# Kernel tuning notes

Measured on AMD Instinct MI355X. Metric: run time of the kernel, lower is better.

The kernel has to match this reference:

```python
import jax, jax.numpy as jnp
import numpy as np

N = 10000
E = 320000
D_IN = 512
D_OUT = 256


def setup_inputs() -> dict:
    key = jax.random.key(0)
    ks = jax.random.split(key, 10)
    x = jax.random.normal(ks[0], (N, D_IN), dtype=jnp.float32)
    edge_index = jax.random.randint(ks[1], (2, E), 0, N, dtype=jnp.int64)
    s_in = 1.0 / np.sqrt(D_IN)
    s_out = 1.0 / np.sqrt(D_OUT)
    W0 = jax.random.uniform(ks[2], (D_IN, D_OUT), minval=-s_in, maxval=s_in, dtype=jnp.float32)
    b0 = jax.random.uniform(ks[3], (D_OUT,), minval=-s_in, maxval=s_in, dtype=jnp.float32)
    Wl1 = jax.random.uniform(ks[4], (D_OUT, D_OUT), minval=-s_out, maxval=s_out, dtype=jnp.float32)
    bl1 = jax.random.uniform(ks[5], (D_OUT,), minval=-s_out, maxval=s_out, dtype=jnp.float32)
    Wr1 = jax.random.uniform(ks[6], (D_OUT, D_OUT), minval=-s_out, maxval=s_out, dtype=jnp.float32)
    Wl2 = jax.random.uniform(ks[7], (D_OUT, D_OUT), minval=-s_out, maxval=s_out, dtype=jnp.float32)
    bl2 = jax.random.uniform(ks[8], (D_OUT,), minval=-s_out, maxval=s_out, dtype=jnp.float32)
    Wr2 = jax.random.uniform(ks[9], (D_OUT, D_OUT), minval=-s_out, maxval=s_out, dtype=jnp.float32)
    return {"x": x, "edge_index": edge_index, "W0": W0, "b0": b0,
            "Wl1": Wl1, "bl1": bl1, "Wr1": Wr1,
            "Wl2": Wl2, "bl2": bl2, "Wr2": Wr2}


def _sage_conv(h, src, dst, Wl, bl, Wr):
    # mean aggregation over incoming edges: msg j->i uses h[src], summed at dst
    msg = h[src]                                        # [E, D]
    agg = jax.ops.segment_sum(msg, dst, num_segments=N)  # [N, D]
    deg = jax.ops.segment_sum(jnp.ones((msg.shape[0],), h.dtype), dst, num_segments=N)
    mean = agg / jnp.maximum(deg, 1.0)[:, None]
    return mean @ Wl + bl + h @ Wr


def reference(x, edge_index, W0, b0, Wl1, bl1, Wr1, Wl2, bl2, Wr2):
    src, dst = edge_index[0], edge_index[1]
    h = x @ W0 + b0                 # lin; dropout = identity (eval mode)
    out1 = jax.nn.relu(_sage_conv(h, src, dst, Wl1, bl1, Wr1)) + h
    out2 = _sage_conv(out1, src, dst, Wl2, bl2, Wr2) + out1
    return (out1, out2)
```

## Files before the change

### kernel.cpp

```cpp
#include <hip/hip_runtime.h>
#include <cstdint>

#define N_NODES 10000
#define N_EDGES 320000
#define DIN 512
#define DOUT 256
#define DEG_CAP 96

using short8 = __attribute__((ext_vector_type(8))) short;
using f32x4  = __attribute__((ext_vector_type(4))) float;
typedef unsigned short ushort_t;

static __device__ __forceinline__ unsigned short f2bf(float f) {
  unsigned u = __builtin_bit_cast(unsigned, f);
  u += 0x7fffu + ((u >> 16) & 1u);
  return (unsigned short)(u >> 16);
}
static __device__ __forceinline__ float bf2f(unsigned short s) {
  unsigned u = ((unsigned)s) << 16;
  return __builtin_bit_cast(float, u);
}

static __device__ __forceinline__ int detect64(const unsigned* ei) {
  unsigned z = 0;
  #pragma unroll
  for (int i = 1; i < 32; i += 2) z |= ei[i];
  return z == 0u;
}
static __device__ __forceinline__ int load_idx(const unsigned* ei, int i, int is64) {
  return is64 ? (int)ei[2 * i] : (int)ei[i];
}

#define B_EDGE 1250
#define B_W    1536
#define B_X    5000
__global__ __launch_bounds__(256) void prep_all(
    const unsigned* __restrict__ ei, int* __restrict__ cnt,
    int* __restrict__ srcs,
    const float* __restrict__ x, ushort_t* __restrict__ xb,
    const float* __restrict__ W0,
    const float* __restrict__ Wl1, const float* __restrict__ Wr1,
    const float* __restrict__ Wl2, const float* __restrict__ Wr2,
    ushort_t* __restrict__ W0T, ushort_t* __restrict__ WT1,
    ushort_t* __restrict__ WT2) {
  int b = blockIdx.x;
  if (b < B_EDGE) {
    int is64 = detect64(ei);
    int e = b * 256 + threadIdx.x;
    int d = load_idx(ei, N_EDGES + e, is64);
    int s = load_idx(ei, e, is64);
    int pos = atomicAdd(&cnt[d], 1);
    if (pos < DEG_CAP) srcs[d * DEG_CAP + pos] = s;
  } else if (b < B_EDGE + B_W) {
    int g = (b - B_EDGE) * 256 + threadIdx.x;
    int mat = g >> 17;
    int r = g & 131071;
    int n = r >> 9, k = r & 511;
    float v;
    ushort_t* dst;
    if (mat == 0)      { v = W0[k * 256 + n]; dst = W0T; }
    else if (mat == 1) { v = (k < 256) ? Wl1[k * 256 + n] : Wr1[(k - 256) * 256 + n]; dst = WT1; }
    else               { v = (k < 256) ? Wl2[k * 256 + n] : Wr2[(k - 256) * 256 + n]; dst = WT2; }
    dst[r] = f2bf(v);
  } else {
    int g = (b - B_EDGE - B_W) * 256 + threadIdx.x;
    float4 f = *(const float4*)(x + (size_t)g * 4);
    uint2 o;
    o.x = (unsigned)f2bf(f.x) | ((unsigned)f2bf(f.y) << 16);
    o.y = (unsigned)f2bf(f.z) | ((unsigned)f2bf(f.w) << 16);
    *(uint2*)(xb + (size_t)g * 4) = o;
  }
}

__global__ __launch_bounds__(256) void agg_mean(const ushort_t* __restrict__ h,
                                                const int* __restrict__ cnt,
                                                const int* __restrict__ srcs,
                                                ushort_t* __restrict__ mean) {
  int node = blockIdx.x * 4 + (threadIdx.x >> 6);
  int lane = threadIdx.x & 63;
  if (node >= N_NODES) return;
  int deg = cnt[node];
  int d = (deg < DEG_CAP) ? deg : DEG_CAP;
  int beg = node * DEG_CAP;
  int end = beg + d;
  float a0 = 0.f, a1 = 0.f, a2 = 0.f, a3 = 0.f;
  int j = beg;
  for (; j + 8 <= end; j += 8) {
    int4 sa = *(const int4*)(srcs + j);
    int4 sb = *(const int4*)(srcs + j + 4);
    uint2 u0 = *(const uint2*)(h + (size_t)sa.x * 256 + lane * 4);
    uint2 u1 = *(const uint2*)(h + (size_t)sa.y * 256 + lane * 4);
    uint2 u2 = *(const uint2*)(h + (size_t)sa.z * 256 + lane * 4);
    uint2 u3 = *(const uint2*)(h + (size_t)sa.w * 256 + lane * 4);
    uint2 u4 = *(const uint2*)(h + (size_t)sb.x * 256 + lane * 4);
    uint2 u5 = *(const uint2*)(h + (size_t)sb.y * 256 + lane * 4);
    uint2 u6 = *(const uint2*)(h + (size_t)sb.z * 256 + lane * 4);
    uint2 u7 = *(const uint2*)(h + (size_t)sb.w * 256 + lane * 4);
    a0 += bf2f(u0.x & 0xffff) + bf2f(u1.x & 0xffff) + bf2f(u2.x & 0xffff) + bf2f(u3.x & 0xffff);
    a1 += bf2f(u0.x >> 16)    + bf2f(u1.x >> 16)    + bf2f(u2.x >> 16)    + bf2f(u3.x >> 16);
    a2 += bf2f(u0.y & 0xffff) + bf2f(u1.y & 0xffff) + bf2f(u2.y & 0xffff) + bf2f(u3.y & 0xffff);
    a3 += bf2f(u0.y >> 16)    + bf2f(u1.y >> 16)    + bf2f(u2.y >> 16)    + bf2f(u3.y >> 16);
    a0 += bf2f(u4.x & 0xffff) + bf2f(u5.x & 0xffff) + bf2f(u6.x & 0xffff) + bf2f(u7.x & 0xffff);
    a1 += bf2f(u4.x >> 16)    + bf2f(u5.x >> 16)    + bf2f(u6.x >> 16)    + bf2f(u7.x >> 16);
    a2 += bf2f(u4.y & 0xffff) + bf2f(u5.y & 0xffff) + bf2f(u6.y & 0xffff) + bf2f(u7.y & 0xffff);
    a3 += bf2f(u4.y >> 16)    + bf2f(u5.y >> 16)    + bf2f(u6.y >> 16)    + bf2f(u7.y >> 16);
  }
  for (; j + 4 <= end; j += 4) {
    int4 s4 = *(const int4*)(srcs + j);
    uint2 u0 = *(const uint2*)(h + (size_t)s4.x * 256 + lane * 4);
    uint2 u1 = *(const uint2*)(h + (size_t)s4.y * 256 + lane * 4);
    uint2 u2 = *(const uint2*)(h + (size_t)s4.z * 256 + lane * 4);
    uint2 u3 = *(const uint2*)(h + (size_t)s4.w * 256 + lane * 4);
    a0 += bf2f(u0.x & 0xffff) + bf2f(u1.x & 0xffff) + bf2f(u2.x & 0xffff) + bf2f(u3.x & 0xffff);
    a1 += bf2f(u0.x >> 16)    + bf2f(u1.x >> 16)    + bf2f(u2.x >> 16)    + bf2f(u3.x >> 16);
    a2 += bf2f(u0.y & 0xffff) + bf2f(u1.y & 0xffff) + bf2f(u2.y & 0xffff) + bf2f(u3.y & 0xffff);
    a3 += bf2f(u0.y >> 16)    + bf2f(u1.y >> 16)    + bf2f(u2.y >> 16)    + bf2f(u3.y >> 16);
  }
  for (; j < end; ++j) {
    int s0 = srcs[j];
    uint2 u0 = *(const uint2*)(h + (size_t)s0 * 256 + lane * 4);
    a0 += bf2f(u0.x & 0xffff);
    a1 += bf2f(u0.x >> 16);
    a2 += bf2f(u0.y & 0xffff);
    a3 += bf2f(u0.y >> 16);
  }
  float inv = 1.0f / (float)(d > 1 ? d : 1);
  a0 *= inv; a1 *= inv; a2 *= inv; a3 *= inv;
  uint2 o;
  o.x = (unsigned)f2bf(a0) | ((unsigned)f2bf(a1) << 16);
  o.y = (unsigned)f2bf(a2) | ((unsigned)f2bf(a3) << 16);
  *(uint2*)(mean + (size_t)node * 256 + lane * 4) = o;
}

template<int DO_RELU, int HAS_ADD, int HAS_OUTF, int HAS_OUTB, int SPLIT_A>
__global__ __launch_bounds__(256) void gemm_pan(
    const ushort_t* __restrict__ A0, const ushort_t* __restrict__ A1,
    const ushort_t* __restrict__ BT, const float* __restrict__ bias,
    const ushort_t* __restrict__ addB,
    float* __restrict__ outF, ushort_t* __restrict__ outB, int M) {
  __shared__ ushort_t Bs[64 * 520];

  const int bid = blockIdx.x;
  const int sg  = bid >> 5;
  const int r32 = bid & 31;
  const int xt  = (sg << 3) + (r32 & 7);
  const int yt  = r32 >> 3;
  const int xtiles = (M + 127) >> 7;
  if (xt >= xtiles) return;

  const int tid  = threadIdx.x;
  const int lane = tid & 63;
  const int w    = tid >> 6;
  const int bn   = yt * 64;
  const int mbase = xt * 128 + w * 32;

  #pragma unroll
  for (int i = 0; i < 16; ++i) {
    int c = i * 256 + tid;
    int row = c >> 6;
    int c8  = (c & 63) * 8;
    uint4 bv = *(const uint4*)(BT + (size_t)(bn + row) * 512 + c8);
    *(uint4*)&Bs[row * 520 + c8] = bv;
  }
  __syncthreads();

  f32x4 acc[2][4] = {};
  const int mrow = lane & 15;
  const int k8   = (lane >> 4) * 8;

  #pragma unroll
  for (int kt = 0; kt < 512; kt += 32) {
    const ushort_t* Asrc;
    int acol, ald;
    if (SPLIT_A) {
      if (kt < 256) { Asrc = A0; acol = kt; } else { Asrc = A1; acol = kt - 256; }
      ald = 256;
    } else {
      Asrc = A0; acol = kt; ald = 512;
    }
    short8 a[2], b[4];
    #pragma unroll
    for (int s = 0; s < 2; ++s) {
      int row = mbase + s * 16 + mrow;
      a[s] = *(const short8*)(Asrc + (size_t)row * ald + acol + k8);
    }
    #pragma unroll
    for (int ni = 0; ni < 4; ++ni)
      b[ni] = *(const short8*)&Bs[(ni * 16 + mrow) * 520 + kt + k8];
    #pragma unroll
    for (int s = 0; s < 2; ++s)
      #pragma unroll
      for (int ni = 0; ni < 4; ++ni)
        acc[s][ni] = __builtin_amdgcn_mfma_f32_16x16x32_bf16(a[s], b[ni], acc[s][ni], 0, 0, 0);
  }

  const int cq   = lane >> 4;
  const int ccol = lane & 15;
  #pragma unroll
  for (int ni = 0; ni < 4; ++ni) {
    int gcol = bn + ni * 16 + ccol;
    float bv = bias[gcol];
    #pragma unroll
    for (int s = 0; s < 2; ++s) {
      #pragma unroll
      for (int r = 0; r < 4; ++r) {
        int grow = mbase + s * 16 + cq * 4 + r;
        if (grow < M) {
          float v = acc[s][ni][r] + bv;
          if (DO_RELU) v = fmaxf(v, 0.f);
          if (HAS_ADD) v += bf2f(addB[(size_t)grow * DOUT + gcol]);
          if (HAS_OUTF) __builtin_nontemporal_store(v, &outF[(size_t)grow * DOUT + gcol]);
          if (HAS_OUTB) outB[(size_t)grow * DOUT + gcol] = f2bf(v);
        }
      }
    }
  }
}

extern "C" void kernel_launch(void* const* d_in, const int* in_sizes, int n_in,
                              void* d_out, int out_size, void* d_ws, size_t ws_size,
                              hipStream_t stream) {
  const float*    x   = (const float*)d_in[0];
  const unsigned* ei  = (const unsigned*)d_in[1];
  const float*    W0  = (const float*)d_in[2];
  const float*    b0  = (const float*)d_in[3];
  const float*    Wl1 = (const float*)d_in[4];
  const float*    bl1 = (const float*)d_in[5];
  const float*    Wr1 = (const float*)d_in[6];
  const float*    Wl2 = (const float*)d_in[7];
  const float*    bl2 = (const float*)d_in[8];
  const float*    Wr2 = (const float*)d_in[9];

  char* ws = (char*)d_ws;
  size_t off = 0;
  auto alloc = [&](size_t bytes) {
    char* p = ws + off;
    off += (bytes + 255) & ~(size_t)255;
    return p;
  };
  ushort_t* xb  = (ushort_t*)alloc((size_t)N_NODES * 512 * 2);
  ushort_t* hb  = (ushort_t*)alloc((size_t)N_NODES * 256 * 2);
  ushort_t* o1b = (ushort_t*)alloc((size_t)N_NODES * 256 * 2);
  ushort_t* mb  = (ushort_t*)alloc((size_t)N_NODES * 256 * 2);
  ushort_t* W0T = (ushort_t*)alloc(256 * 512 * 2);
  ushort_t* WT1 = (ushort_t*)alloc(256 * 512 * 2);
  ushort_t* WT2 = (ushort_t*)alloc(256 * 512 * 2);
  int* cnt    = (int*)alloc(N_NODES * 4);
  int* srcs   = (int*)alloc((size_t)N_NODES * DEG_CAP * 4);

  float* out1 = (float*)d_out;
  float* out2 = out1 + (size_t)N_NODES * DOUT;

  hipMemsetAsync(cnt, 0, N_NODES * 4, stream);
  prep_all<<<B_EDGE + B_W + B_X, 256, 0, stream>>>(ei, cnt, srcs, x, xb,
                                                   W0, Wl1, Wr1, Wl2, Wr2,
                                                   W0T, WT1, WT2);

  const int GG = 320;
  gemm_pan<0, 0, 0, 1, 0><<<GG, 256, 0, stream>>>(xb, nullptr, W0T, b0, nullptr,
                                                  nullptr, hb, N_NODES);
  agg_mean<<<(N_NODES + 3) / 4, 256, 0, stream>>>(hb, cnt, srcs, mb);
  gemm_pan<1, 1, 1, 1, 1><<<GG, 256, 0, stream>>>(mb, hb, WT1, bl1, hb,
                                                  out1, o1b, N_NODES);
  agg_mean<<<(N_NODES + 3) / 4, 256, 0, stream>>>(o1b, cnt, srcs, mb);
  gemm_pan<0, 1, 1, 0, 1><<<GG, 256, 0, stream>>>(mb, o1b, WT2, bl2, o1b,
                                                  out2, nullptr, N_NODES);
}
```

Baseline: 196.4 us.

## Overlap aggregation with root-weight GEMM and fuse x bf16 conversion into GEMM

Splits each SAGE layer's fused K=512 GEMM into two K=256 GEMMs. The h@Wr+bias half runs in the same launch as the neighbor mean aggregation, so memory-bound gather blocks and MFMA blocks can share the GPU. It also drops the separate x->bf16 pass by converting fp32 x inside the first GEMM's A load. In exchange it adds an fp32 intermediate buffer t that is written and read back each layer, and the first GEMM now loads A in fp32.

```diff
diff --git a/kernel.cpp b/kernel.cpp
--- a/kernel.cpp
+++ b/kernel.cpp
@@ -6,6 +6,7 @@
 #define DIN 512
 #define DOUT 256
 #define DEG_CAP 96
+#define AGGB 2500
 
 using short8 = __attribute__((ext_vector_type(8))) short;
 using f32x4  = __attribute__((ext_vector_type(4))) float;
@@ -33,16 +34,15 @@
 
 #define B_EDGE 1250
 #define B_W    1536
-#define B_X    5000
 __global__ __launch_bounds__(256) void prep_all(
     const unsigned* __restrict__ ei, int* __restrict__ cnt,
     int* __restrict__ srcs,
-    const float* __restrict__ x, ushort_t* __restrict__ xb,
     const float* __restrict__ W0,
     const float* __restrict__ Wl1, const float* __restrict__ Wr1,
     const float* __restrict__ Wl2, const float* __restrict__ Wr2,
-    ushort_t* __restrict__ W0T, ushort_t* __restrict__ WT1,
-    ushort_t* __restrict__ WT2) {
+    ushort_t* __restrict__ W0T,
+    ushort_t* __restrict__ WlT1, ushort_t* __restrict__ WrT1,
+    ushort_t* __restrict__ WlT2, ushort_t* __restrict__ WrT2) {
   int b = blockIdx.x;
   if (b < B_EDGE) {
     int is64 = detect64(ei);
@@ -51,32 +51,27 @@
     int s = load_idx(ei, e, is64);
     int pos = atomicAdd(&cnt[d], 1);
     if (pos < DEG_CAP) srcs[d * DEG_CAP + pos] = s;
-  } else if (b < B_EDGE + B_W) {
+  } else {
     int g = (b - B_EDGE) * 256 + threadIdx.x;
     int mat = g >> 17;
     int r = g & 131071;
     int n = r >> 9, k = r & 511;
-    float v;
-    ushort_t* dst;
-    if (mat == 0)      { v = W0[k * 256 + n]; dst = W0T; }
-    else if (mat == 1) { v = (k < 256) ? Wl1[k * 256 + n] : Wr1[(k - 256) * 256 + n]; dst = WT1; }
-    else               { v = (k < 256) ? Wl2[k * 256 + n] : Wr2[(k - 256) * 256 + n]; dst = WT2; }
-    dst[r] = f2bf(v);
-  } else {
-    int g = (b - B_EDGE - B_W) * 256 + threadIdx.x;
-    float4 f = *(const float4*)(x + (size_t)g * 4);
-    uint2 o;
-    o.x = (unsigned)f2bf(f.x) | ((unsigned)f2bf(f.y) << 16);
-    o.y = (unsigned)f2bf(f.z) | ((unsigned)f2bf(f.w) << 16);
-    *(uint2*)(xb + (size_t)g * 4) = o;
-  }
-}
-
-__global__ __launch_bounds__(256) void agg_mean(const ushort_t* __restrict__ h,
-                                                const int* __restrict__ cnt,
-                                                const int* __restrict__ srcs,
-                                                ushort_t* __restrict__ mean) {
-  int node = blockIdx.x * 4 + (threadIdx.x >> 6);
+    if (mat == 0) {
+      W0T[n * 512 + k] = f2bf(W0[k * 256 + n]);
+    } else if (mat == 1) {
+      if (k < 256) WlT1[n * 256 + k]         = f2bf(Wl1[k * 256 + n]);
+      else         WrT1[n * 256 + (k - 256)] = f2bf(Wr1[(k - 256) * 256 + n]);
+    } else {
+      if (k < 256) WlT2[n * 256 + k]         = f2bf(Wl2[k * 256 + n]);
+      else         WrT2[n * 256 + (k - 256)] = f2bf(Wr2[(k - 256) * 256 + n]);
+    }
+  }
+}
+
+static __device__ __forceinline__ void agg_body(
+    int bid, const ushort_t* __restrict__ h, const int* __restrict__ cnt,
+    const int* __restrict__ srcs, ushort_t* __restrict__ mean) {
+  int node = bid * 4 + (threadIdx.x >> 6);
   int lane = threadIdx.x & 63;
   if (node >= N_NODES) return;
   int deg = cnt[node];
@@ -132,61 +127,67 @@
   *(uint2*)(mean + (size_t)node * 256 + lane * 4) = o;
 }
 
-template<int DO_RELU, int HAS_ADD, int HAS_OUTF, int HAS_OUTB, int SPLIT_A>
-__global__ __launch_bounds__(256) void gemm_pan(
-    const ushort_t* __restrict__ A0, const ushort_t* __restrict__ A1,
-    const ushort_t* __restrict__ BT, const float* __restrict__ bias,
-    const ushort_t* __restrict__ addB,
-    float* __restrict__ outF, ushort_t* __restrict__ outB, int M) {
-  __shared__ ushort_t Bs[64 * 520];
-
-  const int bid = blockIdx.x;
-  const int sg  = bid >> 5;
-  const int r32 = bid & 31;
-  const int xt  = (sg << 3) + (r32 & 7);
-  const int yt  = r32 >> 3;
-  const int xtiles = (M + 127) >> 7;
-  if (xt >= xtiles) return;
-
-  const int tid  = threadIdx.x;
+template<int KDIM, int AF32, int HB, int ADDF, int RELU, int RES,
+         int OUTF, int NTF, int OUTB, int ROT>
+static __device__ __forceinline__ void gemm_body(
+    int gbid, const void* __restrict__ Av, const ushort_t* __restrict__ BT,
+    const float* __restrict__ bias, const float* __restrict__ addF,
+    const ushort_t* __restrict__ resB, float* __restrict__ outF,
+    ushort_t* __restrict__ outB, int M, ushort_t* Bs) {
+  constexpr int LDB = KDIM + 8;
+  const int sg = gbid >> 5, r32 = gbid & 31;
+  const int xt = (sg << 3) + ((r32 + ROT) & 7);
+  const int yt = r32 >> 3;
+  if (xt >= ((M + 127) >> 7)) return;
+  const int tid = threadIdx.x;
   const int lane = tid & 63;
-  const int w    = tid >> 6;
-  const int bn   = yt * 64;
+  const int w = tid >> 6;
+  const int bn = yt * 64;
   const int mbase = xt * 128 + w * 32;
 
+  constexpr int CPR = KDIM / 8;
   #pragma unroll
-  for (int i = 0; i < 16; ++i) {
+  for (int i = 0; i < (64 * CPR) / 256; ++i) {
     int c = i * 256 + tid;
-    int row = c >> 6;
-    int c8  = (c & 63) * 8;
-    uint4 bv = *(const uint4*)(BT + (size_t)(bn + row) * 512 + c8);
-    *(uint4*)&Bs[row * 520 + c8] = bv;
+    int row = c / CPR;
+    int c8 = (c % CPR) * 8;
+    uint4 bv = *(const uint4*)(BT + (size_t)(bn + row) * KDIM + c8);
+    *(uint4*)&Bs[row * LDB + c8] = bv;
   }
   __syncthreads();
 
   f32x4 acc[2][4] = {};
   const int mrow = lane & 15;
-  const int k8   = (lane >> 4) * 8;
+  const int k8 = (lane >> 4) * 8;
 
   #pragma unroll
-  for (int kt = 0; kt < 512; kt += 32) {
-    const ushort_t* Asrc;
-    int acol, ald;
-    if (SPLIT_A) {
-      if (kt < 256) { Asrc = A0; acol = kt; } else { Asrc = A1; acol = kt - 256; }
-      ald = 256;
-    } else {
-      Asrc = A0; acol = kt; ald = 512;
-    }
+  for (int kt = 0; kt < KDIM; kt += 32) {
     short8 a[2], b[4];
     #pragma unroll
     for (int s = 0; s < 2; ++s) {
       int row = mbase + s * 16 + mrow;
-      a[s] = *(const short8*)(Asrc + (size_t)row * ald + acol + k8);
+      if (AF32) {
+        const float* Af = (const float*)Av;
+        float4 f0 = {}, f1 = {};
+        if (row < M) {
+          const float* p = Af + (size_t)row * KDIM + kt + k8;
+          f0 = *(const float4*)p;
+          f1 = *(const float4*)(p + 4);
+        }
+        short8 av;
+        av[0] = (short)f2bf(f0.x); av[1] = (short)f2bf(f0.y);
+        av[2] = (short)f2bf(f0.z); av[3] = (short)f2bf(f0.w);
+        av[4] = (short)f2bf(f1.x); av[5] = (short)f2bf(f1.y);
+        av[6] = (short)f2bf(f1.z); av[7] = (short)f2bf(f1.w);
+        a[s] = av;
+      } else {
+        const ushort_t* Ab = (const ushort_t*)Av;
+        a[s] = *(const short8*)(Ab + (size_t)row * KDIM + kt + k8);
+      }
     }
     #pragma unroll
     for (int ni = 0; ni < 4; ++ni)
-      b[ni] = *(const short8*)&Bs[(ni * 16 + mrow) * 520 + kt + k8];
+      b[ni] = *(const short8*)&Bs[(ni * 16 + mrow) * LDB + kt + k8];
     #pragma unroll
     for (int s = 0; s < 2; ++s)
       #pragma unroll
@@ -194,27 +195,67 @@
         acc[s][ni] = __builtin_amdgcn_mfma_f32_16x16x32_bf16(a[s], b[ni], acc[s][ni], 0, 0, 0);
   }
 
-  const int cq   = lane >> 4;
+  const int cq = lane >> 4;
   const int ccol = lane & 15;
   #pragma unroll
   for (int ni = 0; ni < 4; ++ni) {
     int gcol = bn + ni * 16 + ccol;
-    float bv = bias[gcol];
+    float bv = HB ? bias[gcol] : 0.f;
     #pragma unroll
     for (int s = 0; s < 2; ++s) {
       #pragma unroll
       for (int r = 0; r < 4; ++r) {
         int grow = mbase + s * 16 + cq * 4 + r;
         if (grow < M) {
-          float v = acc[s][ni][r] + bv;
-          if (DO_RELU) v = fmaxf(v, 0.f);
-          if (HAS_ADD) v += bf2f(addB[(size_t)grow * DOUT + gcol]);
-          if (HAS_OUTF) __builtin_nontemporal_store(v, &outF[(size_t)grow * DOUT + gcol]);
-          if (HAS_OUTB) outB[(size_t)grow * DOUT + gcol] = f2bf(v);
+          size_t idx = (size_t)grow * DOUT + gcol;
+          float v = acc[s][ni][r];
+          if (HB)   v += bv;
+          if (ADDF) v += addF[idx];
+          if (RELU) v = fmaxf(v, 0.f);
+          if (RES)  v += bf2f(resB[idx]);
+          if (OUTF) {
+            if (NTF) __builtin_nontemporal_store(v, &outF[idx]);
+            else     outF[idx] = v;
+          }
+          if (OUTB) outB[idx] = f2bf(v);
         }
       }
     }
   }
+}
+
+__global__ __launch_bounds__(256) void gemm1_k(
+    const float* __restrict__ x, const ushort_t* __restrict__ W0T,
+    const float* __restrict__ b0, ushort_t* __restrict__ hb) {
+  __shared__ ushort_t Bs[64 * 520];
+  gemm_body<512, 1, 1, 0, 0, 0, 0, 0, 1, 0>(blockIdx.x, x, W0T, b0, nullptr,
+                                            nullptr, nullptr, hb, N_NODES, Bs);
+}
+
+__global__ __launch_bounds__(256) void combo_k(
+    const ushort_t* __restrict__ h, const int* __restrict__ cnt,
+    const int* __restrict__ srcs, ushort_t* __restrict__ mean,
+    const ushort_t* __restrict__ BT, const float* __restrict__ bias,
+    float* __restrict__ t) {
+  __shared__ ushort_t Bs[64 * 264];
+  if (blockIdx.x < AGGB) {
+    agg_body(blockIdx.x, h, cnt, srcs, mean);
+  } else {
+    gemm_body<256, 0, 1, 0, 0, 0, 1, 0, 0, 4>(blockIdx.x - AGGB, h, BT, bias,
+                                              nullptr, nullptr, t, nullptr,
+                                              N_NODES, Bs);
+  }
+}
+
+template<int RELU, int OUTB>
+__global__ __launch_bounds__(256) void gemmL_k(
+    const ushort_t* __restrict__ A, const ushort_t* __restrict__ BT,
+    const float* __restrict__ t, const ushort_t* __restrict__ res,
+    float* __restrict__ outF, ushort_t* __restrict__ outB) {
+  __shared__ ushort_t Bs[64 * 264];
+  gemm_body<256, 0, 0, 1, RELU, 1, 1, 1, OUTB, 0>(blockIdx.x, A, BT, nullptr,
+                                                  t, res, outF, outB,
+                                                  N_NODES, Bs);
 }
 
 extern "C" void kernel_launch(void* const* d_in, const int* in_sizes, int n_in,
@@ -238,31 +279,28 @@
     off += (bytes + 255) & ~(size_t)255;
     return p;
   };
-  ushort_t* xb  = (ushort_t*)alloc((size_t)N_NODES * 512 * 2);
-  ushort_t* hb  = (ushort_t*)alloc((size_t)N_NODES * 256 * 2);
-  ushort_t* o1b = (ushort_t*)alloc((size_t)N_NODES * 256 * 2);
-  ushort_t* mb  = (ushort_t*)alloc((size_t)N_NODES * 256 * 2);
-  ushort_t* W0T = (ushort_t*)alloc(256 * 512 * 2);
-  ushort_t* WT1 = (ushort_t*)alloc(256 * 512 * 2);
-  ushort_t* WT2 = (ushort_t*)alloc(256 * 512 * 2);
-  int* cnt    = (int*)alloc(N_NODES * 4);
-  int* srcs   = (int*)alloc((size_t)N_NODES * DEG_CAP * 4);
+  ushort_t* hb   = (ushort_t*)alloc((size_t)N_NODES * 256 * 2);
+  ushort_t* o1b  = (ushort_t*)alloc((size_t)N_NODES * 256 * 2);
+  ushort_t* mb   = (ushort_t*)alloc((size_t)N_NODES * 256 * 2);
+  float*    t    = (float*)   alloc((size_t)N_NODES * 256 * 4);
+  ushort_t* W0T  = (ushort_t*)alloc(256 * 512 * 2);
+  ushort_t* WlT1 = (ushort_t*)alloc(256 * 256 * 2);
+  ushort_t* WrT1 = (ushort_t*)alloc(256 * 256 * 2);
+  ushort_t* WlT2 = (ushort_t*)alloc(256 * 256 * 2);
+  ushort_t* WrT2 = (ushort_t*)alloc(256 * 256 * 2);
+  int* cnt  = (int*)alloc(N_NODES * 4);
+  int* srcs = (int*)alloc((size_t)N_NODES * DEG_CAP * 4);
 
   float* out1 = (float*)d_out;
   float* out2 = out1 + (size_t)N_NODES * DOUT;
 
   hipMemsetAsync(cnt, 0, N_NODES * 4, stream);
-  prep_all<<<B_EDGE + B_W + B_X, 256, 0, stream>>>(ei, cnt, srcs, x, xb,
-                                                   W0, Wl1, Wr1, Wl2, Wr2,
-                                                   W0T, WT1, WT2);
-
-  const int GG = 320;
-  gemm_pan<0, 0, 0, 1, 0><<<GG, 256, 0, stream>>>(xb, nullptr, W0T, b0, nullptr,
-                                                  nullptr, hb, N_NODES);
-  agg_mean<<<(N_NODES + 3) / 4, 256, 0, stream>>>(hb, cnt, srcs, mb);
-  gemm_pan<1, 1, 1, 1, 1><<<GG, 256, 0, stream>>>(mb, hb, WT1, bl1, hb,
-                                                  out1, o1b, N_NODES);
-  agg_mean<<<(N_NODES + 3) / 4, 256, 0, stream>>>(o1b, cnt, srcs, mb);
-  gemm_pan<0, 1, 1, 0, 1><<<GG, 256, 0, stream>>>(mb, o1b, WT2, bl2, o1b,
-                                                  out2, nullptr, N_NODES);
-}
+  prep_all<<<B_EDGE + B_W, 256, 0, stream>>>(ei, cnt, srcs,
+                                             W0, Wl1, Wr1, Wl2, Wr2,
+                                             W0T, WlT1, WrT1, WlT2, WrT2);
+  gemm1_k<<<320, 256, 0, stream>>>(x, W0T, b0, hb);
+  combo_k<<<AGGB + 320, 256, 0, stream>>>(hb, cnt, srcs, mb, WrT1, bl1, t);
+  gemmL_k<1, 1><<<320, 256, 0, stream>>>(mb, WlT1, t, hb, out1, o1b);
+  combo_k<<<AGGB + 320, 256, 0, stream>>>(o1b, cnt, srcs, mb, WrT2, bl2, t);
+  gemmL_k<0, 0><<<320, 256, 0, stream>>>(mb, WlT2, t, o1b, out2, nullptr);
+}
```

New measurement: 217.7 us. 10.8% more time.

## Split mean aggregation across two column halves and deepen gather unroll

Applied to the files above, without the earlier changes.

The aggregation kernel now launches twice as many blocks, and each wave handles one 128-column half of a node's feature row with 4-byte loads instead of 8-byte loads. The main loop is unrolled to 16 neighbours so more independent gathers are in flight, and the neighbour index lists are read with nontemporal loads. The goal is more parallelism and memory-level concurrency for the latency-bound gather. The cost is that each index list is read twice and each gather transaction is narrower. The node bounds check was removed; this is safe only because N is divisible by 4.

```diff
diff --git a/kernel.cpp b/kernel.cpp
--- a/kernel.cpp
+++ b/kernel.cpp
@@ -9,6 +9,7 @@
 
 using short8 = __attribute__((ext_vector_type(8))) short;
 using f32x4  = __attribute__((ext_vector_type(4))) float;
+using i32x4  = __attribute__((ext_vector_type(4))) int;
 typedef unsigned short ushort_t;
 
 static __device__ __forceinline__ unsigned short f2bf(float f) {
@@ -76,60 +77,67 @@
                                                 const int* __restrict__ cnt,
                                                 const int* __restrict__ srcs,
                                                 ushort_t* __restrict__ mean) {
-  int node = blockIdx.x * 4 + (threadIdx.x >> 6);
+  int bid  = blockIdx.x;
+  int half = bid >= 2500;
+  int grp  = half ? bid - 2500 : bid;
+  int node = grp * 4 + (threadIdx.x >> 6);
   int lane = threadIdx.x & 63;
-  if (node >= N_NODES) return;
+  int off  = half * 128 + lane * 2;
   int deg = cnt[node];
   int d = (deg < DEG_CAP) ? deg : DEG_CAP;
   int beg = node * DEG_CAP;
   int end = beg + d;
-  float a0 = 0.f, a1 = 0.f, a2 = 0.f, a3 = 0.f;
+  float a0 = 0.f, a1 = 0.f;
   int j = beg;
-  for (; j + 8 <= end; j += 8) {
-    int4 sa = *(const int4*)(srcs + j);
-    int4 sb = *(const int4*)(srcs + j + 4);
-    uint2 u0 = *(const uint2*)(h + (size_t)sa.x * 256 + lane * 4);
-    uint2 u1 = *(const uint2*)(h + (size_t)sa.y * 256 + lane * 4);
-    uint2 u2 = *(const uint2*)(h + (size_t)sa.z * 256 + lane * 4);
-    uint2 u3 = *(const uint2*)(h + (size_t)sa.w * 256 + lane * 4);
-    uint2 u4 = *(const uint2*)(h + (size_t)sb.x * 256 + lane * 4);
-    uint2 u5 = *(const uint2*)(h + (size_t)sb.y * 256 + lane * 4);
-    uint2 u6 = *(const uint2*)(h + (size_t)sb.z * 256 + lane * 4);
-    uint2 u7 = *(const uint2*)(h + (size_t)sb.w * 256 + lane * 4);
-    a0 += bf2f(u0.x & 0xffff) + bf2f(u1.x & 0xffff) + bf2f(u2.x & 0xffff) + bf2f(u3.x & 0xffff);
-    a1 += bf2f(u0.x >> 16)    + bf2f(u1.x >> 16)    + bf2f(u2.x >> 16)    + bf2f(u3.x >> 16);
-    a2 += bf2f(u0.y & 0xffff) + bf2f(u1.y & 0xffff) + bf2f(u2.y & 0xffff) + bf2f(u3.y & 0xffff);
-    a3 += bf2f(u0.y >> 16)    + bf2f(u1.y >> 16)    + bf2f(u2.y >> 16)    + bf2f(u3.y >> 16);
-    a0 += bf2f(u4.x & 0xffff) + bf2f(u5.x & 0xffff) + bf2f(u6.x & 0xffff) + bf2f(u7.x & 0xffff);
-    a1 += bf2f(u4.x >> 16)    + bf2f(u5.x >> 16)    + bf2f(u6.x >> 16)    + bf2f(u7.x >> 16);
-    a2 += bf2f(u4.y & 0xffff) + bf2f(u5.y & 0xffff) + bf2f(u6.y & 0xffff) + bf2f(u7.y & 0xffff);
-    a3 += bf2f(u4.y >> 16)    + bf2f(u5.y >> 16)    + bf2f(u6.y >> 16)    + bf2f(u7.y >> 16);
+  for (; j + 16 <= end; j += 16) {
+    i32x4 sa = __builtin_nontemporal_load((const i32x4*)(srcs + j));
+    i32x4 sb = __builtin_nontemporal_load((const i32x4*)(srcs + j + 4));
+    i32x4 sc = __builtin_nontemporal_load((const i32x4*)(srcs + j + 8));
+    i32x4 sd = __builtin_nontemporal_load((const i32x4*)(srcs + j + 12));
+    unsigned u0 = *(const unsigned*)(h + (size_t)sa[0] * 256 + off);
+    unsigned u1 = *(const unsigned*)(h + (size_t)sa[1] * 256 + off);
+    unsigned u2 = *(const unsigned*)(h + (size_t)sa[2] * 256 + off);
+    unsigned u3 = *(const unsigned*)(h + (size_t)sa[3] * 256 + off);
+    unsigned u4 = *(const unsigned*)(h + (size_t)sb[0] * 256 + off);
+    unsigned u5 = *(const unsigned*)(h + (size_t)sb[1] * 256 + off);
+    unsigned u6 = *(const unsigned*)(h + (size_t)sb[2] * 256 + off);
+    unsigned u7 = *(const unsigned*)(h + (size_t)sb[3] * 256 + off);
+    unsigned u8 = *(const unsigned*)(h + (size_t)sc[0] * 256 + off);
+    unsigned u9 = *(const unsigned*)(h + (size_t)sc[1] * 256 + off);
+    unsigned ua = *(const unsigned*)(h + (size_t)sc[2] * 256 + off);
+    unsigned ub = *(const unsigned*)(h + (size_t)sc[3] * 256 + off);
+    unsigned uc = *(const unsigned*)(h + (size_t)sd[0] * 256 + off);
+    unsigned ud = *(const unsigned*)(h + (size_t)sd[1] * 256 + off);
+    unsigned ue = *(const unsigned*)(h + (size_t)sd[2] * 256 + off);
+    unsigned uf = *(const unsigned*)(h + (size_t)sd[3] * 256 + off);
+    a0 += bf2f(u0 & 0xffff) + bf2f(u1 & 0xffff) + bf2f(u2 & 0xffff) + bf2f(u3 & 0xffff);
+    a1 += bf2f(u0 >> 16)    + bf2f(u1 >> 16)    + bf2f(u2 >> 16)    + bf2f(u3 >> 16);
+    a0 += bf2f(u4 & 0xffff) + bf2f(u5 & 0xffff) + bf2f(u6 & 0xffff) + bf2f(u7 & 0xffff);
+    a1 += bf2f(u4 >> 16)    + bf2f(u5 >> 16)    + bf2f(u6 >> 16)    + bf2f(u7 >> 16);
+    a0 += bf2f(u8 & 0xffff) + bf2f(u9 & 0xffff) + bf2f(ua & 0xffff) + bf2f(ub & 0xffff);
+    a1 += bf2f(u8 >> 16)    + bf2f(u9 >> 16)    + bf2f(ua >> 16)    + bf2f(ub >> 16);
+    a0 += bf2f(uc & 0xffff) + bf2f(ud & 0xffff) + bf2f(ue & 0xffff) + bf2f(uf & 0xffff);
+    a1 += bf2f(uc >> 16)    + bf2f(ud >> 16)    + bf2f(ue >> 16)    + bf2f(uf >> 16);
   }
   for (; j + 4 <= end; j += 4) {
-    int4 s4 = *(const int4*)(srcs + j);
-    uint2 u0 = *(const uint2*)(h + (size_t)s4.x * 256 + lane * 4);
-    uint2 u1 = *(const uint2*)(h + (size_t)s4.y * 256 + lane * 4);
-    uint2 u2 = *(const uint2*)(h + (size_t)s4.z * 256 + lane * 4);
-    uint2 u3 = *(const uint2*)(h + (size_t)s4.w * 256 + lane * 4);
-    a0 += bf2f(u0.x & 0xffff) + bf2f(u1.x & 0xffff) + bf2f(u2.x & 0xffff) + bf2f(u3.x & 0xffff);
-    a1 += bf2f(u0.x >> 16)    + bf2f(u1.x >> 16)    + bf2f(u2.x >> 16)    + bf2f(u3.x >> 16);
-    a2 += bf2f(u0.y & 0xffff) + bf2f(u1.y & 0xffff) + bf2f(u2.y & 0xffff) + bf2f(u3.y & 0xffff);
-    a3 += bf2f(u0.y >> 16)    + bf2f(u1.y >> 16)    + bf2f(u2.y >> 16)    + bf2f(u3.y >> 16);
+    i32x4 s4 = __builtin_nontemporal_load((const i32x4*)(srcs + j));
+    unsigned u0 = *(const unsigned*)(h + (size_t)s4[0] * 256 + off);
+    unsigned u1 = *(const unsigned*)(h + (size_t)s4[1] * 256 + off);
+    unsigned u2 = *(const unsigned*)(h + (size_t)s4[2] * 256 + off);
+    unsigned u3 = *(const unsigned*)(h + (size_t)s4[3] * 256 + off);
+    a0 += bf2f(u0 & 0xffff) + bf2f(u1 & 0xffff) + bf2f(u2 & 0xffff) + bf2f(u3 & 0xffff);
+    a1 += bf2f(u0 >> 16)    + bf2f(u1 >> 16)    + bf2f(u2 >> 16)    + bf2f(u3 >> 16);
   }
   for (; j < end; ++j) {
     int s0 = srcs[j];
-    uint2 u0 = *(const uint2*)(h + (size_t)s0 * 256 + lane * 4);
-    a0 += bf2f(u0.x & 0xffff);
-    a1 += bf2f(u0.x >> 16);
-    a2 += bf2f(u0.y & 0xffff);
-    a3 += bf2f(u0.y >> 16);
+    unsigned u0 = *(const unsigned*)(h + (size_t)s0 * 256 + off);
+    a0 += bf2f(u0 & 0xffff);
+    a1 += bf2f(u0 >> 16);
   }
   float inv = 1.0f / (float)(d > 1 ? d : 1);
-  a0 *= inv; a1 *= inv; a2 *= inv; a3 *= inv;
-  uint2 o;
-  o.x = (unsigned)f2bf(a0) | ((unsigned)f2bf(a1) << 16);
-  o.y = (unsigned)f2bf(a2) | ((unsigned)f2bf(a3) << 16);
-  *(uint2*)(mean + (size_t)node * 256 + lane * 4) = o;
+  a0 *= inv; a1 *= inv;
+  unsigned o = (unsigned)f2bf(a0) | ((unsigned)f2bf(a1) << 16);
+  *(unsigned*)(mean + (size_t)node * 256 + off) = o;
 }
 
 template<int DO_RELU, int HAS_ADD, int HAS_OUTF, int HAS_OUTB, int SPLIT_A>
@@ -259,10 +267,10 @@
   const int GG = 320;
   gemm_pan<0, 0, 0, 1, 0><<<GG, 256, 0, stream>>>(xb, nullptr, W0T, b0, nullptr,
                                                   nullptr, hb, N_NODES);
-  agg_mean<<<(N_NODES + 3) / 4, 256, 0, stream>>>(hb, cnt, srcs, mb);
+  agg_mean<<<5000, 256, 0, stream>>>(hb, cnt, srcs, mb);
   gemm_pan<1, 1, 1, 1, 1><<<GG, 256, 0, stream>>>(mb, hb, WT1, bl1, hb,
                                                   out1, o1b, N_NODES);
-  agg_mean<<<(N_NODES + 3) / 4, 256, 0, stream>>>(o1b, cnt, srcs, mb);
+  agg_mean<<<5000, 256, 0, stream>>>(o1b, cnt, srcs, mb);
   gemm_pan<0, 1, 1, 0, 1><<<GG, 256, 0, stream>>>(mb, o1b, WT2, bl2, o1b,
                                                   out2, nullptr, N_NODES);
 }
```

New measurement: 197.0 us. No clear change (+0.3%).

## Fuse mean aggregation and SAGE GEMM into one persistent kernel with grid barrier

Applied to the files above, without the earlier changes.

Merges each layer's aggregation kernel and GEMM kernel into a single launch. Blocks pull node groups from an atomic ticket counter, and the extra GEMM blocks spin on a done counter before reading the aggregated means. The layer weights are pre-packed into MFMA fragment order so B operands load straight from global memory without LDS staging. The gather loop is also unrolled to 16 and the bf16-to-float conversion simplified. This removes launch gaps and the LDS weight copy, but depends on all blocks being co-resident for the spin barrier to make progress, which risks deadlock or idle waiting.

```diff
diff --git a/kernel.cpp b/kernel.cpp
--- a/kernel.cpp
+++ b/kernel.cpp
@@ -6,6 +6,9 @@
 #define DIN 512
 #define DOUT 256
 #define DEG_CAP 96
+#define NGRP 2500
+#define FG   320
+#define FB   (NGRP + FG)
 
 using short8 = __attribute__((ext_vector_type(8))) short;
 using f32x4  = __attribute__((ext_vector_type(4))) float;
@@ -20,6 +23,8 @@
   unsigned u = ((unsigned)s) << 16;
   return __builtin_bit_cast(float, u);
 }
+static __device__ __forceinline__ float lo_f(unsigned u) { return __builtin_bit_cast(float, u << 16); }
+static __device__ __forceinline__ float hi_f(unsigned u) { return __builtin_bit_cast(float, u & 0xffff0000u); }
 
 static __device__ __forceinline__ int detect64(const unsigned* ei) {
   unsigned z = 0;
@@ -55,13 +60,22 @@
     int g = (b - B_EDGE) * 256 + threadIdx.x;
     int mat = g >> 17;
     int r = g & 131071;
-    int n = r >> 9, k = r & 511;
-    float v;
-    ushort_t* dst;
-    if (mat == 0)      { v = W0[k * 256 + n]; dst = W0T; }
-    else if (mat == 1) { v = (k < 256) ? Wl1[k * 256 + n] : Wr1[(k - 256) * 256 + n]; dst = WT1; }
-    else               { v = (k < 256) ? Wl2[k * 256 + n] : Wr2[(k - 256) * 256 + n]; dst = WT2; }
-    dst[r] = f2bf(v);
+    if (mat == 0) {
+      int n = r >> 9, k = r & 511;
+      W0T[r] = f2bf(W0[k * 256 + n]);
+    } else {
+      int tile = r >> 9, e2 = r & 511;
+      int l = e2 >> 3, j = e2 & 7;
+      int nb = tile >> 4, kb = tile & 15;
+      int n = nb * 16 + (l & 15);
+      int kk = (l >> 4) * 8 + j;
+      const float* Wl = (mat == 1) ? Wl1 : Wl2;
+      const float* Wr = (mat == 1) ? Wr1 : Wr2;
+      ushort_t* P     = (mat == 1) ? WT1 : WT2;
+      float v = (kb < 8) ? Wl[(kb * 32 + kk) * 256 + n]
+                         : Wr[((kb - 8) * 32 + kk) * 256 + n];
+      P[r] = f2bf(v);
+    }
   } else {
     int g = (b - B_EDGE - B_W) * 256 + threadIdx.x;
     float4 f = *(const float4*)(x + (size_t)g * 4);
@@ -72,22 +86,22 @@
   }
 }
 
-__global__ __launch_bounds__(256) void agg_mean(const ushort_t* __restrict__ h,
-                                                const int* __restrict__ cnt,
-                                                const int* __restrict__ srcs,
-                                                ushort_t* __restrict__ mean) {
-  int node = blockIdx.x * 4 + (threadIdx.x >> 6);
+static __device__ __forceinline__ void agg_group(
+    int grp, const ushort_t* __restrict__ h, const int* __restrict__ cnt,
+    const int* __restrict__ srcs, ushort_t* __restrict__ mean) {
+  int node = grp * 4 + (threadIdx.x >> 6);
   int lane = threadIdx.x & 63;
-  if (node >= N_NODES) return;
   int deg = cnt[node];
   int d = (deg < DEG_CAP) ? deg : DEG_CAP;
   int beg = node * DEG_CAP;
   int end = beg + d;
   float a0 = 0.f, a1 = 0.f, a2 = 0.f, a3 = 0.f;
   int j = beg;
-  for (; j + 8 <= end; j += 8) {
+  for (; j + 16 <= end; j += 16) {
     int4 sa = *(const int4*)(srcs + j);
     int4 sb = *(const int4*)(srcs + j + 4);
+    int4 sc = *(const int4*)(srcs + j + 8);
+    int4 sd = *(const int4*)(srcs + j + 12);
     uint2 u0 = *(const uint2*)(h + (size_t)sa.x * 256 + lane * 4);
     uint2 u1 = *(const uint2*)(h + (size_t)sa.y * 256 + lane * 4);
     uint2 u2 = *(const uint2*)(h + (size_t)sa.z * 256 + lane * 4);
@@ -96,14 +110,30 @@
     uint2 u5 = *(const uint2*)(h + (size_t)sb.y * 256 + lane * 4);
     uint2 u6 = *(const uint2*)(h + (size_t)sb.z * 256 + lane * 4);
     uint2 u7 = *(const uint2*)(h + (size_t)sb.w * 256 + lane * 4);
-    a0 += bf2f(u0.x & 0xffff) + bf2f(u1.x & 0xffff) + bf2f(u2.x & 0xffff) + bf2f(u3.x & 0xffff);
-    a1 += bf2f(u0.x >> 16)    + bf2f(u1.x >> 16)    + bf2f(u2.x >> 16)    + bf2f(u3.x >> 16);
-    a2 += bf2f(u0.y & 0xffff) + bf2f(u1.y & 0xffff) + bf2f(u2.y & 0xffff) + bf2f(u3.y & 0xffff);
-    a3 += bf2f(u0.y >> 16)    + bf2f(u1.y >> 16)    + bf2f(u2.y >> 16)    + bf2f(u3.y >> 16);
-    a0 += bf2f(u4.x & 0xffff) + bf2f(u5.x & 0xffff) + bf2f(u6.x & 0xffff) + bf2f(u7.x & 0xffff);
-    a1 += bf2f(u4.x >> 16)    + bf2f(u5.x >> 16)    + bf2f(u6.x >> 16)    + bf2f(u7.x >> 16);
-    a2 += bf2f(u4.y & 0xffff) + bf2f(u5.y & 0xffff) + bf2f(u6.y & 0xffff) + bf2f(u7.y & 0xffff);
-    a3 += bf2f(u4.y >> 16)    + bf2f(u5.y >> 16)    + bf2f(u6.y >> 16)    + bf2f(u7.y >> 16);
+    uint2 u8 = *(const uint2*)(h + (size_t)sc.x * 256 + lane * 4);
+    uint2 u9 = *(const uint2*)(h + (size_t)sc.y * 256 + lane * 4);
+    uint2 ua = *(const uint2*)(h + (size_t)sc.z * 256 + lane * 4);
+    uint2 ub = *(const uint2*)(h + (size_t)sc.w * 256 + lane * 4);
+    uint2 uc = *(const uint2*)(h + (size_t)sd.x * 256 + lane * 4);
+    uint2 ud = *(const uint2*)(h + (size_t)sd.y * 256 + lane * 4);
+    uint2 ue = *(const uint2*)(h + (size_t)sd.z * 256 + lane * 4);
+    uint2 uf = *(const uint2*)(h + (size_t)sd.w * 256 + lane * 4);
+    a0 += lo_f(u0.x) + lo_f(u1.x) + lo_f(u2.x) + lo_f(u3.x);
+    a1 += hi_f(u0.x) + hi_f(u1.x) + hi_f(u2.x) + hi_f(u3.x);
+    a2 += lo_f(u0.y) + lo_f(u1.y) + lo_f(u2.y) + lo_f(u3.y);
+    a3 += hi_f(u0.y) + hi_f(u1.y) + hi_f(u2.y) + hi_f(u3.y);
+    a0 += lo_f(u4.x) + lo_f(u5.x) + lo_f(u6.x) + lo_f(u7.x);
+    a1 += hi_f(u4.x) + hi_f(u5.x) + hi_f(u6.x) + hi_f(u7.x);
+    a2 += lo_f(u4.y) + lo_f(u5.y) + lo_f(u6.y) + lo_f(u7.y);
+    a3 += hi_f(u4.y) + hi_f(u5.y) + hi_f(u6.y) + hi_f(u7.y);
+    a0 += lo_f(u8.x) + lo_f(u9.x) + lo_f(ua.x) + lo_f(ub.x);
+    a1 += hi_f(u8.x) + hi_f(u9.x) + hi_f(ua.x) + hi_f(ub.x);
+    a2 += lo_f(u8.y) + lo_f(u9.y) + lo_f(ua.y) + lo_f(ub.y);
+    a3 += hi_f(u8.y) + hi_f(u9.y) + hi_f(ua.y) + hi_f(ub.y);
+    a0 += lo_f(uc.x) + lo_f(ud.x) + lo_f(ue.x) + lo_f(uf.x);
+    a1 += hi_f(uc.x) + hi_f(ud.x) + hi_f(ue.x) + hi_f(uf.x);
+    a2 += lo_f(uc.y) + lo_f(ud.y) + lo_f(ue.y) + lo_f(uf.y);
+    a3 += hi_f(uc.y) + hi_f(ud.y) + hi_f(ue.y) + hi_f(uf.y);
   }
   for (; j + 4 <= end; j += 4) {
     int4 s4 = *(const int4*)(srcs + j);
@@ -111,18 +141,18 @@
     uint2 u1 = *(const uint2*)(h + (size_t)s4.y * 256 + lane * 4);
     uint2 u2 = *(const uint2*)(h + (size_t)s4.z * 256 + lane * 4);
     uint2 u3 = *(const uint2*)(h + (size_t)s4.w * 256 + lane * 4);
-    a0 += bf2f(u0.x & 0xffff) + bf2f(u1.x & 0xffff) + bf2f(u2.x & 0xffff) + bf2f(u3.x & 0xffff);
-    a1 += bf2f(u0.x >> 16)    + bf2f(u1.x >> 16)    + bf2f(u2.x >> 16)    + bf2f(u3.x >> 16);
-    a2 += bf2f(u0.y & 0xffff) + bf2f(u1.y & 0xffff) + bf2f(u2.y & 0xffff) + bf2f(u3.y & 0xffff);
-    a3 += bf2f(u0.y >> 16)    + bf2f(u1.y >> 16)    + bf2f(u2.y >> 16)    + bf2f(u3.y >> 16);
+    a0 += lo_f(u0.x) + lo_f(u1.x) + lo_f(u2.x) + lo_f(u3.x);
+    a1 += hi_f(u0.x) + hi_f(u1.x) + hi_f(u2.x) + hi_f(u3.x);
+    a2 += lo_f(u0.y) + lo_f(u1.y) + lo_f(u2.y) + lo_f(u3.y);
+    a3 += hi_f(u0.y) + hi_f(u1.y) + hi_f(u2.y) + hi_f(u3.y);
   }
   for (; j < end; ++j) {
     int s0 = srcs[j];
     uint2 u0 = *(const uint2*)(h + (size_t)s0 * 256 + lane * 4);
-    a0 += bf2f(u0.x & 0xffff);
-    a1 += bf2f(u0.x >> 16);
-    a2 += bf2f(u0.y & 0xffff);
-    a3 += bf2f(u0.y >> 16);
+    a0 += lo_f(u0.x);
+    a1 += hi_f(u0.x);
+    a2 += lo_f(u0.y);
+    a3 += hi_f(u0.y);
   }
   float inv = 1.0f / (float)(d > 1 ? d : 1);
   a0 *= inv; a1 *= inv; a2 *= inv; a3 *= inv;
@@ -132,22 +162,16 @@
   *(uint2*)(mean + (size_t)node * 256 + lane * 4) = o;
 }
 
-template<int DO_RELU, int HAS_ADD, int HAS_OUTF, int HAS_OUTB, int SPLIT_A>
-__global__ __launch_bounds__(256) void gemm_pan(
-    const ushort_t* __restrict__ A0, const ushort_t* __restrict__ A1,
-    const ushort_t* __restrict__ BT, const float* __restrict__ bias,
-    const ushort_t* __restrict__ addB,
-    float* __restrict__ outF, ushort_t* __restrict__ outB, int M) {
+__global__ __launch_bounds__(256) void gemm1_k(
+    const ushort_t* __restrict__ A0, const ushort_t* __restrict__ BT,
+    const float* __restrict__ bias, ushort_t* __restrict__ outB) {
   __shared__ ushort_t Bs[64 * 520];
-
   const int bid = blockIdx.x;
   const int sg  = bid >> 5;
   const int r32 = bid & 31;
   const int xt  = (sg << 3) + (r32 & 7);
   const int yt  = r32 >> 3;
-  const int xtiles = (M + 127) >> 7;
-  if (xt >= xtiles) return;
-
+  if (xt >= ((N_NODES + 127) >> 7)) return;
   const int tid  = threadIdx.x;
   const int lane = tid & 63;
   const int w    = tid >> 6;
@@ -167,22 +191,13 @@
   f32x4 acc[2][4] = {};
   const int mrow = lane & 15;
   const int k8   = (lane >> 4) * 8;
-
   #pragma unroll
   for (int kt = 0; kt < 512; kt += 32) {
-    const ushort_t* Asrc;
-    int acol, ald;
-    if (SPLIT_A) {
-      if (kt < 256) { Asrc = A0; acol = kt; } else { Asrc = A1; acol = kt - 256; }
-      ald = 256;
-    } else {
-      Asrc = A0; acol = kt; ald = 512;
-    }
     short8 a[2], b[4];
     #pragma unroll
     for (int s = 0; s < 2; ++s) {
       int row = mbase + s * 16 + mrow;
-      a[s] = *(const short8*)(Asrc + (size_t)row * ald + acol + k8);
+      a[s] = *(const short8*)(A0 + (size_t)row * 512 + kt + k8);
     }
     #pragma unroll
     for (int ni = 0; ni < 4; ++ni)
@@ -205,12 +220,100 @@
       #pragma unroll
       for (int r = 0; r < 4; ++r) {
         int grow = mbase + s * 16 + cq * 4 + r;
-        if (grow < M) {
+        if (grow < N_NODES)
+          outB[(size_t)grow * DOUT + gcol] = f2bf(acc[s][ni][r] + bv);
+      }
+    }
+  }
+}
+
+template<int DO_RELU, int HAS_OUTB>
+__global__ __launch_bounds__(256) void fused_layer(
+    const ushort_t* __restrict__ h, const int* __restrict__ cnt,
+    const int* __restrict__ srcs, ushort_t* __restrict__ mean,
+    const ushort_t* __restrict__ WP, const float* __restrict__ bias,
+    const ushort_t* __restrict__ addB,
+    float* __restrict__ outF, ushort_t* __restrict__ outB,
+    int* __restrict__ ticket, int* __restrict__ done) {
+  __shared__ int tk;
+  const int tid = threadIdx.x;
+
+  for (;;) {
+    __syncthreads();
+    if (tid == 0) tk = atomicAdd(ticket, 1);
+    __syncthreads();
+    int grp = tk;
+    if (grp >= NGRP) break;
+    agg_group(grp, h, cnt, srcs, mean);
+  }
+  __syncthreads();
+  if (tid == 0) {
+    __threadfence();
+    atomicAdd(done, 1);
+  }
+
+  if (blockIdx.x < NGRP) return;
+  if (tid == 0) {
+    while (__hip_atomic_load(done, __ATOMIC_ACQUIRE, __HIP_MEMORY_SCOPE_AGENT) < FB)
+      __builtin_amdgcn_s_sleep(16);
+    __threadfence();
+  }
+  __syncthreads();
+
+  const int gbid = blockIdx.x - NGRP;
+  const int sg  = gbid >> 5;
+  const int r32 = gbid & 31;
+  const int xt  = (sg << 3) + ((r32 + 4) & 7);
+  const int yt  = r32 >> 3;
+  if (xt >= ((N_NODES + 127) >> 7)) return;
+  const int lane = tid & 63;
+  const int w    = tid >> 6;
+  const int bn   = yt * 64;
+  const int mbase = xt * 128 + w * 32;
+  const int nb   = bn >> 4;
+
+  f32x4 acc[2][4] = {};
+  const int mrow = lane & 15;
+  const int k8   = (lane >> 4) * 8;
+  #pragma unroll
+  for (int kt = 0; kt < 512; kt += 32) {
+    const ushort_t* Asrc;
+    int acol;
+    if (kt < 256) { Asrc = mean; acol = kt; } else { Asrc = h; acol = kt - 256; }
+    short8 a[2], b[4];
+    #pragma unroll
+    for (int s = 0; s < 2; ++s) {
+      int row = mbase + s * 16 + mrow;
+      a[s] = *(const short8*)(Asrc + (size_t)row * 256 + acol + k8);
+    }
+    #pragma unroll
+    for (int ni = 0; ni < 4; ++ni)
+      b[ni] = *(const short8*)(WP + ((size_t)(nb + ni) * 16 + (kt >> 5)) * 512 + lane * 8);
+    #pragma unroll
+    for (int s = 0; s < 2; ++s)
+      #pragma unroll
+      for (int ni = 0; ni < 4; ++ni)
+        acc[s][ni] = __builtin_amdgcn_mfma_f32_16x16x32_bf16(a[s], b[ni], acc[s][ni], 0, 0, 0);
+  }
+
+  const int cq   = lane >> 4;
+  const int ccol = lane & 15;
+  #pragma unroll
+  for (int ni = 0; ni < 4; ++ni) {
+    int gcol = bn + ni * 16 + ccol;
+    float bv = bias[gcol];
+    #pragma unroll
+    for (int s = 0; s < 2; ++s) {
+      #pragma unroll
+      for (int r = 0; r < 4; ++r) {
+        int grow = mbase + s * 16 + cq * 4 + r;
+        if (grow < N_NODES) {
+          size_t idx = (size_t)grow * DOUT + gcol;
           float v = acc[s][ni][r] + bv;
           if (DO_RELU) v = fmaxf(v, 0.f);
-          if (HAS_ADD) v += bf2f(addB[(size_t)grow * DOUT + gcol]);
-          if (HAS_OUTF) __builtin_nontemporal_store(v, &outF[(size_t)grow * DOUT + gcol]);
-          if (HAS_OUTB) outB[(size_t)grow * DOUT + gcol] = f2bf(v);
+          v += bf2f(addB[idx]);
+          __builtin_nontemporal_store(v, &outF[idx]);
+          if (HAS_OUTB) outB[idx] = f2bf(v);
         }
       }
     }
@@ -245,24 +348,25 @@
   ushort_t* W0T = (ushort_t*)alloc(256 * 512 * 2);
   ushort_t* WT1 = (ushort_t*)alloc(256 * 512 * 2);
   ushort_t* WT2 = (ushort_t*)alloc(256 * 512 * 2);
-  int* cnt    = (int*)alloc(N_NODES * 4);
-  int* srcs   = (int*)alloc((size_t)N_NODES * DEG_CAP * 4);
+  int* cnt  = (int*)alloc(N_NODES * 4);
+  int* sync = (int*)alloc(256);
+  int* srcs = (int*)alloc((size_t)N_NODES * DEG_CAP * 4);
+
+  int* tk1 = sync + 0;
+  int* dn1 = sync + 16;
+  int* tk2 = sync + 32;
+  int* dn2 = sync + 48;
 
   float* out1 = (float*)d_out;
   float* out2 = out1 + (size_t)N_NODES * DOUT;
 
-  hipMemsetAsync(cnt, 0, N_NODES * 4, stream);
+  hipMemsetAsync(cnt, 0, (size_t)((char*)sync - (char*)cnt) + 256, stream);
   prep_all<<<B_EDGE + B_W + B_X, 256, 0, stream>>>(ei, cnt, srcs, x, xb,
                                                    W0, Wl1, Wr1, Wl2, Wr2,
                                                    W0T, WT1, WT2);
-
-  const int GG = 320;
-  gemm_pan<0, 0, 0, 1, 0><<<GG, 256, 0, stream>>>(xb, nullptr, W0T, b0, nullptr,
-                                                  nullptr, hb, N_NODES);
-  agg_mean<<<(N_NODES + 3) / 4, 256, 0, stream>>>(hb, cnt, srcs, mb);
-  gemm_pan<1, 1, 1, 1, 1><<<GG, 256, 0, stream>>>(mb, hb, WT1, bl1, hb,
-                                                  out1, o1b, N_NODES);
-  agg_mean<<<(N_NODES + 3) / 4, 256, 0, stream>>>(o1b, cnt, srcs, mb);
-  gemm_pan<0, 1, 1, 0, 1><<<GG, 256, 0, stream>>>(mb, o1b, WT2, bl2, o1b,
-                                                  out2, nullptr, N_NODES);
-}
+  gemm1_k<<<320, 256, 0, stream>>>(xb, W0T, b0, hb);
+  fused_layer<1, 1><<<FB, 256, 0, stream>>>(hb, cnt, srcs, mb, WT1, bl1, hb,
+                                            out1, o1b, tk1, dn1);
+  fused_layer<0, 0><<<FB, 256, 0, stream>>>(o1b, cnt, srcs, mb, WT2, bl2, o1b,
+                                            out2, nullptr, tk2, dn2);
+}
```

After: 409.4 us. +108.4%, slower.
